# Performance work log

Hardware: AMD Instinct MI355X
Metric: run time of the kernel (lower is better)

Reference implementation:

```python
import jax, jax.numpy as jnp
import numpy as np

B, S, D, H = 2, 2048, 1024, 16
DK = D // H
WINDOW = 256


def _make_mask():
    # causal local-window sparsity: attend to j in (i-WINDOW, i]
    i = np.arange(S)[:, None]
    j = np.arange(S)[None, :]
    m = (j <= i) & (i - j < WINDOW)
    return jnp.asarray(m)


def setup_inputs() -> dict:
    key = jax.random.key(0)
    ks = jax.random.split(key, 9)
    sw = 1.0 / np.sqrt(D)
    return {
        "x": jax.random.normal(ks[0], (B, S, D), dtype=jnp.float32),
        "wq": jax.random.normal(ks[1], (D, D), dtype=jnp.float32) * sw,
        "bq": jnp.zeros((D,), dtype=jnp.float32),
        "wk": jax.random.normal(ks[2], (D, D), dtype=jnp.float32) * sw,
        "bk": jnp.zeros((D,), dtype=jnp.float32),
        "wv": jax.random.normal(ks[3], (D, D), dtype=jnp.float32) * sw,
        "bv": jnp.zeros((D,), dtype=jnp.float32),
        "wo": jax.random.normal(ks[4], (D, D), dtype=jnp.float32) * sw,
        "bo": jnp.zeros((D,), dtype=jnp.float32),
        "mask": _make_mask(),
    }


def reference(x, wq, bq, wk, bk, wv, bv, wo, bo, mask):
    b, s, d = x.shape
    # projections (torch Linear: x @ W.T + b), split heads -> [b, h, s, dk]
    def proj(w, bias):
        return (x @ w.T + bias).reshape(b, s, H, DK).transpose(0, 2, 1, 3)

    q = proj(wq, bq)
    k = proj(wk, bk)
    v = proj(wv, bv)

    scores = jnp.einsum("bhqd,bhkd->bhqk", q, k) / jnp.sqrt(jnp.float32(DK))
    scores = jnp.where(mask, scores, -jnp.inf)  # mask broadcasts over b, h
    attn = jax.nn.softmax(scores, axis=-1)
    out = jnp.einsum("bhqk,bhkd->bhqd", attn, v)
    out = out.transpose(0, 2, 1, 3).reshape(b, s, d)
    return out @ wo.T + bo
```

## Files before the change

kernel.cpp:

```cpp
#include <hip/hip_runtime.h>

#define S_LEN 2048
#define DMODEL 1024
#define NHEADS 16
#define WIN 256

typedef unsigned short u16;
typedef unsigned int u32;
typedef __attribute__((ext_vector_type(8))) __bf16 bf16x8;
typedef __attribute__((ext_vector_type(4))) float f32x4;
typedef __attribute__((ext_vector_type(8))) u16 u16x8;
typedef __attribute__((ext_vector_type(4))) u16 u16x4;

__device__ __forceinline__ u16 f2bf(float f) {
  u32 u = __builtin_bit_cast(u32, f);
  u += 0x7fffu + ((u >> 16) & 1u);
  return (u16)(u >> 16);
}

#define GLDS16(g, l) __builtin_amdgcn_global_load_lds( \
    (const __attribute__((address_space(1))) void*)(g), \
    (__attribute__((address_space(3))) void*)(l), 16, 0, 0)

#define BAR() { asm volatile("" ::: "memory"); __builtin_amdgcn_s_barrier(); asm volatile("" ::: "memory"); }
#define VMCNT(n) asm volatile("s_waitcnt vmcnt(" #n ")" ::: "memory")

__global__ __launch_bounds__(256) void cast_all(
    const float* __restrict__ x, const float* __restrict__ wq, const float* __restrict__ wk,
    const float* __restrict__ wv, const float* __restrict__ wo,
    u16* __restrict__ xb, u16* __restrict__ wqb, u16* __restrict__ wkb,
    u16* __restrict__ wvb, u16* __restrict__ wob) {
  const int e = (blockIdx.x * 256 + threadIdx.x) * 4;
  const float* src; u16* dst; int off;
  if (e < (1 << 22)) { src = x; dst = xb; off = e; }
  else {
    int r = e - (1 << 22);
    int seg = r >> 20; off = r & ((1 << 20) - 1);
    src = (seg == 0) ? wq : (seg == 1) ? wk : (seg == 2) ? wv : wo;
    dst = (seg == 0) ? wqb : (seg == 1) ? wkb : (seg == 2) ? wvb : wob;
  }
  float4 v = *(const float4*)(src + off);
  u16x4 o = { f2bf(v.x), f2bf(v.y), f2bf(v.z), f2bf(v.w) };
  *(u16x4*)(dst + off) = o;
}

__global__ __launch_bounds__(256) void gemm_nt(
    const u16* __restrict__ A,
    const u16* __restrict__ B0, const u16* __restrict__ B1, const u16* __restrict__ B2,
    const float* __restrict__ bias0, const float* __restrict__ bias1, const float* __restrict__ bias2,
    u16* __restrict__ C0, u16* __restrict__ C1, u16* __restrict__ C2,
    const int M, const int N, const int K)
{
  const u16* Bt; const float* bias; u16* C;
  if (blockIdx.z == 0)      { Bt = B0; bias = bias0; C = C0; }
  else if (blockIdx.z == 1) { Bt = B1; bias = bias1; C = C1; }
  else                      { Bt = B2; bias = bias2; C = C2; }

  __shared__ u16 As[2][128 * 32];
  __shared__ u16 Bs[2][128 * 32];

  const int t = threadIdx.x;
  const int row0 = blockIdx.x * 128;
  const int col0 = blockIdx.y * 128;
  const int lane = t & 63, lo = lane & 15, hi = lane >> 4;
  const int wv = t >> 6;
  const int wr = (wv >> 1) * 64, wc = (wv & 1) * 64;
  const int sx = lo & 3;

  f32x4 acc[4][4];
  #pragma unroll
  for (int i = 0; i < 4; ++i)
    #pragma unroll
    for (int j = 0; j < 4; ++j) acc[i][j] = (f32x4)0.0f;

  const int NT = K >> 5;

  auto stage = [&](int buf, int kt) {
    const int kof = kt * 32;
    #pragma unroll
    for (int c = 0; c < 2; ++c) {
      const int off = t * 16 + c * 4096;
      const int r = off >> 6;
      const int g = ((off >> 4) & 3) ^ (r & 3);
      GLDS16(A  + (size_t)(row0 + r) * K + (kof + g * 8), (u16*)As + buf * 4096 + (off >> 1));
      GLDS16(Bt + (size_t)(col0 + r) * K + (kof + g * 8), (u16*)Bs + buf * 4096 + (off >> 1));
    }
  };

  stage(0, 0);
  stage(1, 1);
  for (int kt = 0; kt < NT; ++kt) {
    const int cur = kt & 1;
    if (kt + 1 < NT) { VMCNT(4); } else { VMCNT(0); }
    BAR();
    bf16x8 af[4], bfr[4];
    #pragma unroll
    for (int mi = 0; mi < 4; ++mi) {
      const int row = wr + mi * 16 + lo;
      af[mi] = *(const bf16x8*)&As[cur][row * 32 + ((hi ^ sx) << 3)];
    }
    #pragma unroll
    for (int ni = 0; ni < 4; ++ni) {
      const int row = wc + ni * 16 + lo;
      bfr[ni] = *(const bf16x8*)&Bs[cur][row * 32 + ((hi ^ sx) << 3)];
    }
    #pragma unroll
    for (int mi = 0; mi < 4; ++mi)
      #pragma unroll
      for (int ni = 0; ni < 4; ++ni)
        acc[mi][ni] = __builtin_amdgcn_mfma_f32_16x16x32_bf16(af[mi], bfr[ni], acc[mi][ni], 0, 0, 0);
    BAR();
    if (kt + 2 < NT) stage(cur, kt + 2);
  }

  #pragma unroll
  for (int mi = 0; mi < 4; ++mi) {
    #pragma unroll
    for (int ni = 0; ni < 4; ++ni) {
      const int col = col0 + wc + ni * 16 + lo;
      const float bv = bias[col];
      #pragma unroll
      for (int r = 0; r < 4; ++r) {
        const int row = row0 + wr + mi * 16 + hi * 4 + r;
        C[(size_t)row * N + col] = f2bf(acc[mi][ni][r] + bv);
      }
    }
  }
}

__global__ __launch_bounds__(256) void gemm_out64(
    const u16* __restrict__ A, const u16* __restrict__ Bt,
    const float* __restrict__ bias, float* __restrict__ C)
{
  constexpr int N = 1024, K = 1024;

  __shared__ u16 As[2][128 * 32];
  __shared__ u16 Bs[2][64 * 32];

  int id = blockIdx.y * gridDim.x + blockIdx.x;
  int wgid = (id & 7) * 64 + (id >> 3);
  const int row0 = (wgid >> 4) * 128;
  const int col0 = (wgid & 15) * 64;

  const int t = threadIdx.x;
  const int lane = t & 63, lo = lane & 15, hi = lane >> 4;
  const int wv = t >> 6;
  const int wr = (wv >> 1) * 64, wc = (wv & 1) * 32;
  const int sx = lo & 3;

  f32x4 acc[4][2];
  #pragma unroll
  for (int i = 0; i < 4; ++i)
    #pragma unroll
    for (int j = 0; j < 2; ++j) acc[i][j] = (f32x4)0.0f;

  auto stage = [&](int buf, int kt) {
    const int kof = kt * 32;
    #pragma unroll
    for (int c = 0; c < 2; ++c) {
      const int off = t * 16 + c * 4096;
      const int r = off >> 6;
      const int g = ((off >> 4) & 3) ^ (r & 3);
      GLDS16(A + (size_t)(row0 + r) * K + (kof + g * 8), (u16*)As + buf * 4096 + (off >> 1));
    }
    {
      const int off = t * 16;
      const int r = off >> 6;
      const int g = ((off >> 4) & 3) ^ (r & 3);
      GLDS16(Bt + (size_t)(col0 + r) * K + (kof + g * 8), (u16*)Bs + buf * 2048 + (off >> 1));
    }
  };

  stage(0, 0);
  stage(1, 1);
  for (int kt = 0; kt < (K >> 5); ++kt) {
    const int cur = kt & 1;
    if (kt + 1 < (K >> 5)) { VMCNT(3); } else { VMCNT(0); }
    BAR();
    bf16x8 af[4], bfr[2];
    #pragma unroll
    for (int mi = 0; mi < 4; ++mi) {
      const int row = wr + mi * 16 + lo;
      af[mi] = *(const bf16x8*)&As[cur][row * 32 + ((hi ^ sx) << 3)];
    }
    #pragma unroll
    for (int ni = 0; ni < 2; ++ni) {
      const int row = wc + ni * 16 + lo;
      bfr[ni] = *(const bf16x8*)&Bs[cur][row * 32 + ((hi ^ sx) << 3)];
    }
    #pragma unroll
    for (int mi = 0; mi < 4; ++mi)
      #pragma unroll
      for (int ni = 0; ni < 2; ++ni)
        acc[mi][ni] = __builtin_amdgcn_mfma_f32_16x16x32_bf16(af[mi], bfr[ni], acc[mi][ni], 0, 0, 0);
    BAR();
    if (kt + 2 < (K >> 5)) stage(cur, kt + 2);
  }

  #pragma unroll
  for (int mi = 0; mi < 4; ++mi) {
    #pragma unroll
    for (int ni = 0; ni < 2; ++ni) {
      const int col = col0 + wc + ni * 16 + lo;
      const float bv = bias[col];
      #pragma unroll
      for (int r = 0; r < 4; ++r) {
        const int row = row0 + wr + mi * 16 + hi * 4 + r;
        C[(size_t)row * N + col] = acc[mi][ni][r] + bv;
      }
    }
  }
}

__device__ __forceinline__ int swzK(int row, int col) {
  int byte = (row << 7) + (col << 1);
  byte ^= (row & 7) << 4;
  return byte >> 1;
}
__device__ __forceinline__ int swzV(int d, int j) {
  int byte = (d << 7) + (j << 1);
  byte ^= ((d & 7) << 4) ^ (((d >> 4) & 3) << 5);
  return byte >> 1;
}

__global__ __launch_bounds__(512) void attn_win(const u16* __restrict__ Q,
                                                const u16* __restrict__ K,
                                                const u16* __restrict__ V,
                                                u16* __restrict__ O) {
  const int qt = blockIdx.x, h = blockIdx.y, b = blockIdx.z;
  const int q0 = qt * 128;
  const int t = threadIdx.x;
  const int wv = t >> 6, lane = t & 63, lo = lane & 15, hi = lane >> 4;

  __shared__ u16 Ks[2][64 * 64];
  __shared__ u16 Vt[2][64 * 64];
  __shared__ u16 Ps[8][16 * 64];

  const size_t base = ((size_t)b * S_LEN) * DMODEL + h * 64;
  const int w0 = q0 + wv * 16;

  bf16x8 qf[2];
  {
    const u16* qp = Q + base + (size_t)(w0 + lo) * DMODEL;
    u16x8 qa = *(const u16x8*)(qp + hi * 8);
    u16x8 qb = *(const u16x8*)(qp + 32 + hi * 8);
    union { u16x8 s; bf16x8 v; } ua, ub;
    #pragma unroll
    for (int e = 0; e < 8; ++e) {
      float fa = __builtin_bit_cast(float, (u32)qa[e] << 16) * 0.125f;
      float fb = __builtin_bit_cast(float, (u32)qb[e] << 16) * 0.125f;
      ua.s[e] = (u16)(__builtin_bit_cast(u32, fa) >> 16);
      ub.s[e] = (u16)(__builtin_bit_cast(u32, fb) >> 16);
    }
    qf[0] = ua.v; qf[1] = ub.v;
  }

  const int vrow = t >> 3;
  const int vc0  = (t & 7) * 8;
  const int ktmin = max(0, (256 - q0) >> 6);

  u16x8 kra, vra;
  auto issue = [&](int kt) {
    const int jg = q0 - 256 + kt * 64 + vrow;
    if (jg >= 0) {
      kra = *(const u16x8*)(K + base + (size_t)jg * DMODEL + vc0);
      vra = *(const u16x8*)(V + base + (size_t)jg * DMODEL + vc0);
    } else { kra = (u16x8)0; vra = (u16x8)0; }
  };
  auto commit = [&](int buf) {
    *(u16x8*)&Ks[buf][swzK(vrow, vc0)] = kra;
    #pragma unroll
    for (int e = 0; e < 8; ++e)
      Vt[buf][swzV(vc0 + e, vrow)] = vra[e];
  };

  issue(ktmin);
  commit(0);
  __syncthreads();

  f32x4 oacc[4];
  #pragma unroll
  for (int i = 0; i < 4; ++i) oacc[i] = (f32x4)0.0f;
  float l_r[4] = {0.f, 0.f, 0.f, 0.f};

  int cur = 0;
  for (int kt = ktmin; kt < 6; ++kt) {
    const int kstart = q0 - 256 + kt * 64;
    if (kt < 5) issue(kt + 1);

    const bool act = (kstart <= w0 + 15) && (kstart + 63 >= w0 - 255);
    if (act) {
      f32x4 sfr[4];
      #pragma unroll
      for (int ni = 0; ni < 4; ++ni) {
        sfr[ni] = (f32x4)0.0f;
        #pragma unroll
        for (int kq = 0; kq < 2; ++kq) {
          bf16x8 kf = *(const bf16x8*)&Ks[cur][swzK(ni * 16 + lo, kq * 32 + hi * 8)];
          sfr[ni] = __builtin_amdgcn_mfma_f32_16x16x32_bf16(qf[kq], kf, sfr[ni], 0, 0, 0);
        }
      }

      const int i0 = w0 + hi * 4;
      float pr[4][4];
      #pragma unroll
      for (int ni = 0; ni < 4; ++ni) {
        const int j = kstart + ni * 16 + lo;
        #pragma unroll
        for (int r = 0; r < 4; ++r) {
          const int i = i0 + r;
          const bool ok = (j >= 0) & (j <= i) & (i - j < WIN);
          const float x = ok ? sfr[ni][r] : -1e30f;
          const float p = __expf(x);
          pr[ni][r] = p;
          l_r[r] += p;
        }
      }

      #pragma unroll
      for (int ni = 0; ni < 4; ++ni)
        #pragma unroll
        for (int r = 0; r < 4; ++r)
          Ps[wv][swzK(hi * 4 + r, ni * 16 + lo)] = f2bf(pr[ni][r]);

      bf16x8 pa[2];
      #pragma unroll
      for (int kp = 0; kp < 2; ++kp)
        pa[kp] = *(const bf16x8*)&Ps[wv][swzK(lo, kp * 32 + hi * 8)];

      #pragma unroll
      for (int ni = 0; ni < 4; ++ni) {
        #pragma unroll
        for (int kp = 0; kp < 2; ++kp) {
          bf16x8 vf = *(const bf16x8*)&Vt[cur][swzV(ni * 16 + lo, kp * 32 + hi * 8)];
          oacc[ni] = __builtin_amdgcn_mfma_f32_16x16x32_bf16(pa[kp], vf, oacc[ni], 0, 0, 0);
        }
      }
    }

    if (kt < 5) commit(cur ^ 1);
    __syncthreads();
    cur ^= 1;
  }

  #pragma unroll
  for (int d = 1; d < 16; d <<= 1) {
    #pragma unroll
    for (int r = 0; r < 4; ++r) l_r[r] += __shfl_xor(l_r[r], d);
  }

  #pragma unroll
  for (int r = 0; r < 4; ++r) {
    const float inv = 1.0f / l_r[r];
    const int row = w0 + hi * 4 + r;
    #pragma unroll
    for (int ni = 0; ni < 4; ++ni)
      O[base + (size_t)row * DMODEL + ni * 16 + lo] = f2bf(oacc[ni][r] * inv);
  }
}

extern "C" void kernel_launch(void* const* d_in, const int* in_sizes, int n_in,
                              void* d_out, int out_size, void* d_ws, size_t ws_size,
                              hipStream_t stream) {
  const float* x  = (const float*)d_in[0];
  const float* wq = (const float*)d_in[1];
  const float* bq = (const float*)d_in[2];
  const float* wk = (const float*)d_in[3];
  const float* bk = (const float*)d_in[4];
  const float* wvp = (const float*)d_in[5];
  const float* bv = (const float*)d_in[6];
  const float* wo = (const float*)d_in[7];
  const float* bo = (const float*)d_in[8];
  float* out = (float*)d_out;

  char* ws = (char*)d_ws;
  const size_t MB = 1024 * 1024;
  u16* xb  = (u16*)(ws);
  u16* wqb = (u16*)(ws + 8 * MB);
  u16* wkb = (u16*)(ws + 10 * MB);
  u16* wvb = (u16*)(ws + 12 * MB);
  u16* wob = (u16*)(ws + 14 * MB);
  u16* Qb  = (u16*)(ws + 16 * MB);
  u16* Kb  = (u16*)(ws + 24 * MB);
  u16* Vb  = (u16*)(ws + 32 * MB);
  u16* Ob  = (u16*)(ws + 40 * MB);

  cast_all<<<8192, 256, 0, stream>>>(x, wq, wk, wvp, wo, xb, wqb, wkb, wvb, wob);

  dim3 g1(4096 / 128, 1024 / 128, 3);
  gemm_nt<<<g1, 256, 0, stream>>>(xb, wqb, wkb, wvb, bq, bk, bv,
                                  Qb, Kb, Vb, 4096, 1024, 1024);

  attn_win<<<dim3(S_LEN / 128, NHEADS, 2), 512, 0, stream>>>(Qb, Kb, Vb, Ob);

  gemm_out64<<<dim3(32, 16), 256, 0, stream>>>(Ob, wob, bo, out);
}
```

Measured before the change: 81.43 us.

## Stage 128-key tiles with async LDS loads for K and setprio around MFMA

The attention kernel now processes keys in 128-wide tiles, three iterations instead of six, which halves the number of barriers. K is loaded straight into LDS with global_load_lds using an XOR swizzle on the source address, so the K register round-trip goes away. V is still transposed through registers, 16 elements per thread. MFMA sections are wrapped in s_setprio to favour matrix issue. LDS use grows to 32 KB each for K and V, which may reduce occupancy.

```diff
diff --git a/kernel.cpp b/kernel.cpp
--- a/kernel.cpp
+++ b/kernel.cpp
@@ -218,7 +218,7 @@
   return byte >> 1;
 }
 __device__ __forceinline__ int swzV(int d, int j) {
-  int byte = (d << 7) + (j << 1);
+  int byte = (d << 8) + (j << 1);
   byte ^= ((d & 7) << 4) ^ (((d >> 4) & 3) << 5);
   return byte >> 1;
 }
@@ -232,8 +232,8 @@
   const int t = threadIdx.x;
   const int wv = t >> 6, lane = t & 63, lo = lane & 15, hi = lane >> 4;
 
-  __shared__ u16 Ks[2][64 * 64];
-  __shared__ u16 Vt[2][64 * 64];
+  __shared__ u16 Ks[2][128 * 64];
+  __shared__ u16 Vt[2][64 * 128];
   __shared__ u16 Ps[8][16 * 64];
 
   const size_t base = ((size_t)b * S_LEN) * DMODEL + h * 64;
@@ -255,27 +255,38 @@
     qf[0] = ua.v; qf[1] = ub.v;
   }
 
-  const int vrow = t >> 3;
-  const int vc0  = (t & 7) * 8;
-  const int ktmin = max(0, (256 - q0) >> 6);
-
-  u16x8 kra, vra;
-  auto issue = [&](int kt) {
-    const int jg = q0 - 256 + kt * 64 + vrow;
-    if (jg >= 0) {
-      kra = *(const u16x8*)(K + base + (size_t)jg * DMODEL + vc0);
-      vra = *(const u16x8*)(V + base + (size_t)jg * DMODEL + vc0);
-    } else { kra = (u16x8)0; vra = (u16x8)0; }
+  const int ktmin = max(0, (256 - q0) >> 7);
+
+  auto stageK = [&](int buf, int kt) {
+    #pragma unroll
+    for (int c = 0; c < 2; ++c) {
+      const int r = c * 64 + (t >> 3);
+      const int jg = max(0, q0 - 256 + kt * 128 + r);
+      const int g = (t & 7) ^ (r & 7);
+      GLDS16(K + base + (size_t)jg * DMODEL + g * 8,
+             (u16*)Ks + buf * 8192 + c * 4096 + t * 8);
+    }
   };
-  auto commit = [&](int buf) {
-    *(u16x8*)&Ks[buf][swzK(vrow, vc0)] = kra;
-    #pragma unroll
-    for (int e = 0; e < 8; ++e)
-      Vt[buf][swzV(vc0 + e, vrow)] = vra[e];
+
+  const int jr = t >> 2;
+  const int d0 = (t & 3) * 16;
+  u16x8 vra, vrb;
+  auto issueV = [&](int kt) {
+    const int jg = max(0, q0 - 256 + kt * 128 + jr);
+    const u16* sv = V + base + (size_t)jg * DMODEL + d0;
+    vra = *(const u16x8*)sv; vrb = *(const u16x8*)(sv + 8);
   };
-
-  issue(ktmin);
-  commit(0);
+  auto commitV = [&](int buf) {
+    #pragma unroll
+    for (int e = 0; e < 8; ++e) {
+      Vt[buf][swzV(d0 + e, jr)]     = vra[e];
+      Vt[buf][swzV(d0 + 8 + e, jr)] = vrb[e];
+    }
+  };
+
+  stageK(0, ktmin);
+  issueV(ktmin);
+  commitV(0);
   __syncthreads();
 
   f32x4 oacc[4];
@@ -284,28 +295,33 @@
   float l_r[4] = {0.f, 0.f, 0.f, 0.f};
 
   int cur = 0;
-  for (int kt = ktmin; kt < 6; ++kt) {
-    const int kstart = q0 - 256 + kt * 64;
-    if (kt < 5) issue(kt + 1);
-
-    const bool act = (kstart <= w0 + 15) && (kstart + 63 >= w0 - 255);
-    if (act) {
+  for (int kt = ktmin; kt < 3; ++kt) {
+    const int kstart = q0 - 256 + kt * 128;
+    if (kt < 2) { stageK(cur ^ 1, kt + 1); issueV(kt + 1); }
+
+    #pragma unroll
+    for (int jh = 0; jh < 2; ++jh) {
+      const int hstart = kstart + jh * 64;
+      if (hstart > w0 + 15 || hstart + 63 < w0 - 255) continue;
+
       f32x4 sfr[4];
+      __builtin_amdgcn_s_setprio(1);
       #pragma unroll
       for (int ni = 0; ni < 4; ++ni) {
         sfr[ni] = (f32x4)0.0f;
         #pragma unroll
         for (int kq = 0; kq < 2; ++kq) {
-          bf16x8 kf = *(const bf16x8*)&Ks[cur][swzK(ni * 16 + lo, kq * 32 + hi * 8)];
+          bf16x8 kf = *(const bf16x8*)&Ks[cur][swzK(jh * 64 + ni * 16 + lo, kq * 32 + hi * 8)];
           sfr[ni] = __builtin_amdgcn_mfma_f32_16x16x32_bf16(qf[kq], kf, sfr[ni], 0, 0, 0);
         }
       }
+      __builtin_amdgcn_s_setprio(0);
 
       const int i0 = w0 + hi * 4;
       float pr[4][4];
       #pragma unroll
       for (int ni = 0; ni < 4; ++ni) {
-        const int j = kstart + ni * 16 + lo;
+        const int j = hstart + ni * 16 + lo;
         #pragma unroll
         for (int r = 0; r < 4; ++r) {
           const int i = i0 + r;
@@ -328,17 +344,19 @@
       for (int kp = 0; kp < 2; ++kp)
         pa[kp] = *(const bf16x8*)&Ps[wv][swzK(lo, kp * 32 + hi * 8)];
 
+      __builtin_amdgcn_s_setprio(1);
       #pragma unroll
       for (int ni = 0; ni < 4; ++ni) {
         #pragma unroll
         for (int kp = 0; kp < 2; ++kp) {
-          bf16x8 vf = *(const bf16x8*)&Vt[cur][swzV(ni * 16 + lo, kp * 32 + hi * 8)];
+          bf16x8 vf = *(const bf16x8*)&Vt[cur][swzV(ni * 16 + lo, jh * 64 + kp * 32 + hi * 8)];
           oacc[ni] = __builtin_amdgcn_mfma_f32_16x16x32_bf16(pa[kp], vf, oacc[ni], 0, 0, 0);
         }
       }
-    }
-
-    if (kt < 5) commit(cur ^ 1);
+      __builtin_amdgcn_s_setprio(0);
+    }
+
+    if (kt < 2) commitV(cur ^ 1);
     __syncthreads();
     cur ^= 1;
   }
```

After: 86.61 us. 6.4% more time.
